# Performance work log

Measured on AMD Instinct MI355X. Metric: run time of the kernel, lower is better.

## Reference

```python
import jax, jax.numpy as jnp
import numpy as np

B, T, E, H = 4, 1024, 512, 8
DH = E // H  # head dim = 64


def setup_inputs() -> dict:
    key = jax.random.key(0)
    ks = jax.random.split(key, 6)
    s = 1.0 / np.sqrt(E)
    return {
        "q": jax.random.normal(ks[0], (B, T, E), dtype=jnp.float32),
        "kv": jax.random.normal(ks[1], (B, T, E), dtype=jnp.float32),
        "Wq": jax.random.normal(ks[2], (E, E), dtype=jnp.float32) * s,
        "Wk": jax.random.normal(ks[3], (E, E), dtype=jnp.float32) * s,
        "Wv": jax.random.normal(ks[4], (E, E), dtype=jnp.float32) * s,
        "Wo": jax.random.normal(ks[5], (E, E), dtype=jnp.float32) * s,
        "head_num": H,
    }


def _split_heads_dh(x, h):
    # einops 'b t (d h)' with h=head_num: head index is FASTEST in channel dim
    b, t, e = x.shape
    d = e // h
    return x.reshape(b, t, d, h).transpose(0, 3, 1, 2)  # (b, h, t, d)


def reference(q, kv, Wq, Wk, Wv, Wo, head_num):
    e = q.shape[-1]
    dk = (e // head_num) ** 0.5  # NOTE: multiplied, per original code

    qp = q @ Wq   # weights stored as (in, out); Linear(bias=False)
    kp = kv @ Wk
    vp = kv @ Wv

    query = _split_heads_dh(qp, head_num)  # (b, h, t, d)
    key = _split_heads_dh(kp, head_num)
    value = _split_heads_dh(vp, head_num)

    qf = jnp.fft.fftn(query, axes=(-2, -1))  # complex, over (t, d)
    kf = jnp.fft.fftn(key, axes=(-2, -1))

    # complex einsum, key NOT conjugated (faithful to torch source)
    energy = jnp.einsum("bhid,bhjd->bhij", qf, kf) * dk
    energy = jnp.fft.ifftn(energy, axes=(-2, -1)).real  # (b, h, t, t)

    attention = jax.nn.softmax(energy, axis=-1)
    out = jnp.einsum("bhij,bhjd->bhid", attention, value)  # (b, h, t, d)

    # einops 'b h t d -> b t (h d)': head index SLOWEST in output channel dim
    b, h, t, d = out.shape
    out = out.transpose(0, 2, 1, 3).reshape(b, t, h * d)
    return out @ Wo
```

## Files before the change

### kernel.cpp

```cpp
#include <hip/hip_runtime.h>
#include <math.h>

#define BB 4
#define TT 1024
#define EE 512
#define HH 8
#define DD 64
#define BT (BB * TT)

typedef _Float16 f16;
typedef __attribute__((ext_vector_type(8))) _Float16 f16x8;
typedef __attribute__((ext_vector_type(4))) float f32x4;

__global__ __launch_bounds__(256) void prep_k(
    const float* __restrict__ q, const float* __restrict__ kv,
    const float* __restrict__ Wq, const float* __restrict__ Wk,
    const float* __restrict__ Wv, const float* __restrict__ Wo,
    f16* __restrict__ wqh, f16* __restrict__ wql,
    f16* __restrict__ wkh, f16* __restrict__ wkl,
    f16* __restrict__ wvh, f16* __restrict__ woh,
    f16* __restrict__ qAhi, f16* __restrict__ qAlo,
    f16* __restrict__ kvAhi, f16* __restrict__ kvAlo) {
    const int t = threadIdx.x;
    const int y = blockIdx.y;
    if (y < 4) {
        int idx = blockIdx.x * 256 + t;
        int k = idx & (EE - 1);
        int n = idx >> 9;
        if (y == 0) {
            float v = Wq[k * EE + n] * 512.0f;
            f16 hi = (f16)v;
            wqh[n * EE + k] = hi;
            wql[n * EE + k] = (f16)(v - (float)hi);
        } else if (y == 1) {
            int d = n >> 3, h = n & 7;
            int sn = (((DD - d) & (DD - 1)) << 3) | h;
            float v = Wk[k * EE + sn];
            f16 hi = (f16)v;
            wkh[n * EE + k] = hi;
            wkl[n * EE + k] = (f16)(v - (float)hi);
        } else if (y == 2) {
            wvh[n * EE + k] = (f16)Wv[k * EE + n];
        } else {
            woh[n * EE + k] = (f16)Wo[k * EE + n];
        }
    } else {
        const float* src = (y == 4) ? q : kv;
        f16* dh = (y == 4) ? qAhi : kvAhi;
        f16* dl = (y == 4) ? qAlo : kvAlo;
        int base = (blockIdx.x * 256 + t) * 8;
        float4 a = *(const float4*)&src[base];
        float4 c = *(const float4*)&src[base + 4];
        float xs[8] = {a.x, a.y, a.z, a.w, c.x, c.y, c.z, c.w};
        f16x8 hi, lo;
#pragma unroll
        for (int e = 0; e < 8; ++e) {
            f16 hh = (f16)xs[e];
            hi[e] = hh;
            lo[e] = (f16)(xs[e] - (float)hh);
        }
        *(f16x8*)&dh[base] = hi;
        *(f16x8*)&dl[base] = lo;
    }
}

__global__ __launch_bounds__(256) void proj_k(
    const f16* __restrict__ qAhi, const f16* __restrict__ qAlo,
    const f16* __restrict__ kvAhi, const f16* __restrict__ kvAlo,
    const f16* __restrict__ wqh, const f16* __restrict__ wql,
    const f16* __restrict__ wkh, const f16* __restrict__ wkl,
    const f16* __restrict__ wvh,
    f16* __restrict__ qhi, f16* __restrict__ qlo,
    f16* __restrict__ khi, f16* __restrict__ klo, f16* __restrict__ vP) {
    __shared__ __align__(16) f16 Ah_s[2][128][40];
    __shared__ __align__(16) f16 Al_s[2][128][40];
    __shared__ __align__(16) f16 Wh_s[2][64][40];
    __shared__ __align__(16) f16 Wl_s[2][64][40];
    __shared__ __align__(16) f16 Wv_s[2][64][40];
    f16 (*Ep)[136] = reinterpret_cast<f16(*)[136]>(&Ah_s[0][0][0]);

    const int t = threadIdx.x;
    const int w = t >> 6, l = t & 63;
    const int wm = w >> 1, wn = w & 1;
    const int fr = l & 15, fc = l >> 4;
    const int m0b = blockIdx.x * 128;
    const int n0b = blockIdx.y * 64;
    const int z   = blockIdx.z;
    const int ar = t >> 1, ak = t & 1;
    const int wr = t >> 2, wc = t & 3;

    const f16* AH = z ? kvAhi : qAhi;
    const f16* AL = z ? kvAlo : qAlo;
    const f16* WH = z ? wkh : wqh;
    const f16* WL = z ? wkl : wql;

    f32x4 accK[4][2], accV[4][2];
#pragma unroll
    for (int i = 0; i < 4; ++i)
#pragma unroll
        for (int j = 0; j < 2; ++j) {
            accK[i][j] = f32x4{0.f, 0.f, 0.f, 0.f};
            accV[i][j] = f32x4{0.f, 0.f, 0.f, 0.f};
        }

    f16x8 ah8[2], al8[2], wh8, wl8, wv8;

    auto loadAB = [&](int k0) {
        size_t aoff = (size_t)(m0b + ar) * EE + k0 + ak * 16;
        ah8[0] = *(const f16x8*)&AH[aoff];
        ah8[1] = *(const f16x8*)&AH[aoff + 8];
        al8[0] = *(const f16x8*)&AL[aoff];
        al8[1] = *(const f16x8*)&AL[aoff + 8];
        size_t woff = (size_t)(n0b + wr) * EE + k0 + wc * 8;
        wh8 = *(const f16x8*)&WH[woff];
        wl8 = *(const f16x8*)&WL[woff];
        if (z) wv8 = *(const f16x8*)&wvh[woff];
    };
    auto stage = [&](int bf) {
        *(f16x8*)&Ah_s[bf][ar][ak * 16]     = ah8[0];
        *(f16x8*)&Ah_s[bf][ar][ak * 16 + 8] = ah8[1];
        *(f16x8*)&Al_s[bf][ar][ak * 16]     = al8[0];
        *(f16x8*)&Al_s[bf][ar][ak * 16 + 8] = al8[1];
        *(f16x8*)&Wh_s[bf][wr][wc * 8] = wh8;
        *(f16x8*)&Wl_s[bf][wr][wc * 8] = wl8;
        if (z) *(f16x8*)&Wv_s[bf][wr][wc * 8] = wv8;
    };

    loadAB(0);
    stage(0);
    __syncthreads();
    int cur = 0;
    for (int ks = 0; ks < 16; ++ks) {
        if (ks < 15) loadAB((ks + 1) * 32);
        f16x8 Ahf[4], Alf[4], Bh[2], Bl[2], Bv[2];
#pragma unroll
        for (int mi = 0; mi < 4; ++mi) {
            Ahf[mi] = *(const f16x8*)&Ah_s[cur][wm * 64 + mi * 16 + fr][fc * 8];
            Alf[mi] = *(const f16x8*)&Al_s[cur][wm * 64 + mi * 16 + fr][fc * 8];
        }
#pragma unroll
        for (int nj = 0; nj < 2; ++nj) {
            Bh[nj] = *(const f16x8*)&Wh_s[cur][wn * 32 + nj * 16 + fr][fc * 8];
            Bl[nj] = *(const f16x8*)&Wl_s[cur][wn * 32 + nj * 16 + fr][fc * 8];
            if (z) Bv[nj] = *(const f16x8*)&Wv_s[cur][wn * 32 + nj * 16 + fr][fc * 8];
        }
        __builtin_amdgcn_s_setprio(1);
#pragma unroll
        for (int mi = 0; mi < 4; ++mi)
#pragma unroll
            for (int nj = 0; nj < 2; ++nj) {
                accK[mi][nj] = __builtin_amdgcn_mfma_f32_16x16x32_f16(
                    Ahf[mi], Bh[nj], accK[mi][nj], 0, 0, 0);
                accK[mi][nj] = __builtin_amdgcn_mfma_f32_16x16x32_f16(
                    Ahf[mi], Bl[nj], accK[mi][nj], 0, 0, 0);
                accK[mi][nj] = __builtin_amdgcn_mfma_f32_16x16x32_f16(
                    Alf[mi], Bh[nj], accK[mi][nj], 0, 0, 0);
                if (z)
                    accV[mi][nj] = __builtin_amdgcn_mfma_f32_16x16x32_f16(
                        Ahf[mi], Bv[nj], accV[mi][nj], 0, 0, 0);
            }
        __builtin_amdgcn_s_setprio(0);
        if (ks < 15) stage(cur ^ 1);
        __syncthreads();
        cur ^= 1;
    }

    f16* dsthi = z ? khi : qhi;
    f16* dstlo = z ? klo : qlo;
#pragma unroll
    for (int mi = 0; mi < 4; ++mi)
#pragma unroll
        for (int nj = 0; nj < 2; ++nj)
#pragma unroll
            for (int r = 0; r < 4; ++r)
                Ep[wn * 32 + nj * 16 + fr][wm * 64 + mi * 16 + fc * 4 + r] =
                    (f16)accK[mi][nj][r];
    __syncthreads();
#pragma unroll
    for (int i = 0; i < 4; ++i) {
        int task = t * 4 + i;
        int mr = task >> 3, h = task & 7;
        f16x8 v;
#pragma unroll
        for (int d = 0; d < 8; ++d) v[d] = Ep[8 * d + h][mr];
        *(f16x8*)&dsthi[((size_t)h * BT + m0b + mr) * DD + (n0b >> 3)] = v;
    }
    __syncthreads();
#pragma unroll
    for (int mi = 0; mi < 4; ++mi)
#pragma unroll
        for (int nj = 0; nj < 2; ++nj)
#pragma unroll
            for (int r = 0; r < 4; ++r) {
                float x = accK[mi][nj][r];
                f16 hh = (f16)x;
                Ep[wn * 32 + nj * 16 + fr][wm * 64 + mi * 16 + fc * 4 + r] =
                    (f16)(x - (float)hh);
            }
    __syncthreads();
#pragma unroll
    for (int i = 0; i < 4; ++i) {
        int task = t * 4 + i;
        int mr = task >> 3, h = task & 7;
        f16x8 v;
#pragma unroll
        for (int d = 0; d < 8; ++d) v[d] = Ep[8 * d + h][mr];
        *(f16x8*)&dstlo[((size_t)h * BT + m0b + mr) * DD + (n0b >> 3)] = v;
    }
    if (z) {
        __syncthreads();
#pragma unroll
        for (int mi = 0; mi < 4; ++mi)
#pragma unroll
            for (int nj = 0; nj < 2; ++nj)
#pragma unroll
                for (int r = 0; r < 4; ++r)
                    Ep[wn * 32 + nj * 16 + fr][wm * 64 + mi * 16 + fc * 4 + r] =
                        (f16)accV[mi][nj][r];
        __syncthreads();
#pragma unroll
        for (int i = 0; i < 4; ++i) {
            int task = t * 4 + i;
            int mg = task & 15, nn = task >> 4;
            int h = nn & 7, dl = nn >> 3;
            int d = (n0b >> 3) + dl;
            int koff = m0b + mg * 8;
            int tile = koff >> 6;
            int kf   = (koff >> 5) & 1;
            int lg2  = (koff >> 3) & 3;
            int dvt  = d >> 4, lqd = d & 15;
            f16x8 v = *(const f16x8*)&Ep[nn][mg * 8];
            size_t off = (((((size_t)h * 64 + tile) * 2 + kf) * 4 + dvt) * 64 +
                          lg2 * 16 + lqd) * 8;
            *(f16x8*)&vP[off] = v;
        }
    }
}

__global__ __launch_bounds__(256) void outmm_k(const f16* __restrict__ Af,
                                               const f16* __restrict__ WThi,
                                               float* __restrict__ out) {
    __shared__ __align__(16) f16 Ah_s[2][64][72];
    __shared__ __align__(16) f16 Wh_s[2][64][72];

    const int t = threadIdx.x;
    const int w = t >> 6, l = t & 63;
    const int wm = w >> 1, wn = w & 1;
    const int fr = l & 15, fc = l >> 4;
    const int m0b = blockIdx.x * 64;
    const int n0b = blockIdx.y * 64;
    const int sr = t >> 2, sch = t & 3;

    f32x4 acc[2][2];
#pragma unroll
    for (int i = 0; i < 2; ++i)
#pragma unroll
        for (int j = 0; j < 2; ++j) acc[i][j] = f32x4{0.f, 0.f, 0.f, 0.f};

    f16x8 af[2], wf[2];
    auto loadAB = [&](int k0) {
#pragma unroll
        for (int i = 0; i < 2; ++i) {
            af[i] = *(const f16x8*)&Af[(size_t)(m0b + sr) * EE + k0 + sch * 16 + i * 8];
            wf[i] = *(const f16x8*)&WThi[(size_t)(n0b + sr) * EE + k0 + sch * 16 + i * 8];
        }
    };
    auto stage = [&](int bf) {
#pragma unroll
        for (int i = 0; i < 2; ++i) {
            *(f16x8*)&Ah_s[bf][sr][sch * 16 + i * 8] = af[i];
            *(f16x8*)&Wh_s[bf][sr][sch * 16 + i * 8] = wf[i];
        }
    };

    loadAB(0);
    stage(0);
    __syncthreads();
    int cur = 0;
    for (int ks = 0; ks < 8; ++ks) {
        if (ks < 7) loadAB((ks + 1) * 64);
        f16x8 Ahf[2][2], Bhf[2][2];
#pragma unroll
        for (int mi = 0; mi < 2; ++mi)
#pragma unroll
            for (int kb = 0; kb < 2; ++kb)
                Ahf[mi][kb] =
                    *(const f16x8*)&Ah_s[cur][wm * 32 + mi * 16 + fr][kb * 32 + fc * 8];
#pragma unroll
        for (int nj = 0; nj < 2; ++nj)
#pragma unroll
            for (int kb = 0; kb < 2; ++kb)
                Bhf[nj][kb] =
                    *(const f16x8*)&Wh_s[cur][wn * 32 + nj * 16 + fr][kb * 32 + fc * 8];
        __builtin_amdgcn_s_setprio(1);
#pragma unroll
        for (int mi = 0; mi < 2; ++mi)
#pragma unroll
            for (int nj = 0; nj < 2; ++nj)
#pragma unroll
                for (int kb = 0; kb < 2; ++kb)
                    acc[mi][nj] = __builtin_amdgcn_mfma_f32_16x16x32_f16(
                        Ahf[mi][kb], Bhf[nj][kb], acc[mi][nj], 0, 0, 0);
        __builtin_amdgcn_s_setprio(0);
        if (ks < 7) stage(cur ^ 1);
        __syncthreads();
        cur ^= 1;
    }

#pragma unroll
    for (int mi = 0; mi < 2; ++mi)
#pragma unroll
        for (int nj = 0; nj < 2; ++nj)
#pragma unroll
            for (int r = 0; r < 4; ++r)
                out[(size_t)(m0b + wm * 32 + mi * 16 + fc * 4 + r) * EE +
                    n0b + wn * 32 + nj * 16 + fr] = acc[mi][nj][r];
}

__global__ __launch_bounds__(256) void attn_mfma_k(const f16* __restrict__ qhiP,
    const f16* __restrict__ qloP, const f16* __restrict__ khiP,
    const f16* __restrict__ kloP, const f16* __restrict__ vP,
    f16* __restrict__ ctx) {
    __shared__ __align__(16) f16 Khi[2][64][64];
    __shared__ __align__(16) f16 Klo[2][64][64];
    __shared__ __align__(16) f16 Pl[4][16][88];

    const int bid = blockIdx.x;
    const int swz = (bid & 7) * 64 + (bid >> 3);
    const int bx = swz & 15;
    const int h  = (swz >> 4) & 7;
    const int b  = swz >> 7;

    const int t  = threadIdx.x;
    const int w  = t >> 6;
    const int l  = t & 63;
    const int lg = l >> 4;
    const int lq = l & 15;
    const int q0 = bx * 64 + w * 16;
    const size_t plane = ((size_t)h * BT + (size_t)b * TT) * DD;

    f16x8 Qhi[2], Qlo[2];
#pragma unroll
    for (int kf = 0; kf < 2; ++kf) {
        size_t qo = plane + (size_t)(q0 + lq) * DD + kf * 32 + lg * 8;
        Qhi[kf] = *(const f16x8*)&qhiP[qo];
        Qlo[kf] = *(const f16x8*)&qloP[qo];
    }

    f32x4 Oacc[4];
#pragma unroll
    for (int i = 0; i < 4; ++i) Oacc[i] = f32x4{0.f, 0.f, 0.f, 0.f};
    float m = -1e30f, lsum = 0.f;

    const int sr = t >> 2, sch = t & 3;
    f16x8 kh[2], kl[2];

    auto loadK = [&](int kt0) {
        size_t off = plane + (size_t)(kt0 + sr) * DD + sch * 16;
        kh[0] = *(const f16x8*)&khiP[off];
        kh[1] = *(const f16x8*)&khiP[off + 8];
        kl[0] = *(const f16x8*)&kloP[off];
        kl[1] = *(const f16x8*)&kloP[off + 8];
    };
    auto stageK = [&](int bf) {
#pragma unroll
        for (int i = 0; i < 2; ++i) {
            int chunk = sch * 2 + i;
            int dsw = chunk ^ (sr & 7);
            *(f16x8*)&Khi[bf][sr][dsw * 8] = kh[i];
            *(f16x8*)&Klo[bf][sr][dsw * 8] = kl[i];
        }
    };

    loadK(0);
    stageK(0);
    __syncthreads();
    int cur = 0;

    for (int kt0 = 0; kt0 < TT; kt0 += 64) {
        const f16* tb = vP + ((size_t)h * 64 + ((b * TT + kt0) >> 6)) * 4096;
        f16x8 bv[2][4];
#pragma unroll
        for (int kf = 0; kf < 2; ++kf)
#pragma unroll
            for (int dvt = 0; dvt < 4; ++dvt)
                bv[kf][dvt] = *(const f16x8*)&tb[((kf * 4 + dvt) * 64 + l) * 8];
        if (kt0 + 64 < TT) loadK(kt0 + 64);

        f32x4 Sc[4];
        __builtin_amdgcn_s_setprio(1);
#pragma unroll
        for (int kt = 0; kt < 4; ++kt) {
            f32x4 c = f32x4{0.f, 0.f, 0.f, 0.f};
            int keyr = kt * 16 + lq;
#pragma unroll
            for (int kf = 0; kf < 2; ++kf) {
                int dblk = kf * 4 + lg;
                int sw = dblk ^ (keyr & 7);
                f16x8 ahi = *(const f16x8*)&Khi[cur][keyr][sw * 8];
                f16x8 alo = *(const f16x8*)&Klo[cur][keyr][sw * 8];
                c = __builtin_amdgcn_mfma_f32_16x16x32_f16(ahi, Qhi[kf], c, 0, 0, 0);
                c = __builtin_amdgcn_mfma_f32_16x16x32_f16(ahi, Qlo[kf], c, 0, 0, 0);
                c = __builtin_amdgcn_mfma_f32_16x16x32_f16(alo, Qhi[kf], c, 0, 0, 0);
            }
            Sc[kt] = c;
        }
        __builtin_amdgcn_s_setprio(0);

        float sv[16];
#pragma unroll
        for (int kt = 0; kt < 4; ++kt)
#pragma unroll
            for (int r = 0; r < 4; ++r) sv[kt * 4 + r] = Sc[kt][r];
        float tm = sv[0];
#pragma unroll
        for (int i = 1; i < 16; ++i) tm = fmaxf(tm, sv[i]);
        tm = fmaxf(tm, __shfl_xor(tm, 16));
        tm = fmaxf(tm, __shfl_xor(tm, 32));

        bool skip = __all(tm <= m + 8.0f);
        float Mn = m, corr = 1.0f;
        if (!skip) {
            Mn = fmaxf(m, tm);
            corr = __expf(m - Mn);
        }
        float ps = 0.f;
        f16 ph[16];
#pragma unroll
        for (int i = 0; i < 16; ++i) {
            float p = __expf(sv[i] - Mn);
            ps += p;
            ph[i] = (f16)p;
        }
        ps += __shfl_xor(ps, 16);
        ps += __shfl_xor(ps, 32);
        if (skip) {
            lsum += ps;
        } else {
            lsum = lsum * corr + ps;
            m = Mn;
        }

#pragma unroll
        for (int kt = 0; kt < 4; ++kt)
#pragma unroll
            for (int rp = 0; rp < 4; rp += 2) {
                union { f16 h; unsigned short u; } u0, u1;
                u0.h = ph[kt * 4 + rp]; u1.h = ph[kt * 4 + rp + 1];
                unsigned int pk = ((unsigned int)u1.u << 16) | u0.u;
                *(unsigned int*)&Pl[w][lq][kt * 16 + lg * 4 + rp] = pk;
            }

        if (!skip) {
            float cq[4];
#pragma unroll
            for (int r = 0; r < 4; ++r) cq[r] = __shfl(corr, lg * 4 + r);
#pragma unroll
            for (int dvt = 0; dvt < 4; ++dvt)
#pragma unroll
                for (int r = 0; r < 4; ++r) Oacc[dvt][r] *= cq[r];
        }

        __builtin_amdgcn_s_setprio(1);
#pragma unroll
        for (int kf = 0; kf < 2; ++kf) {
            f16x8 pa = *(const f16x8*)&Pl[w][lq][kf * 32 + lg * 8];
#pragma unroll
            for (int dvt = 0; dvt < 4; ++dvt)
                Oacc[dvt] = __builtin_amdgcn_mfma_f32_16x16x32_f16(
                    pa, bv[kf][dvt], Oacc[dvt], 0, 0, 0);
        }
        __builtin_amdgcn_s_setprio(0);

        if (kt0 + 64 < TT) stageK(cur ^ 1);
        __syncthreads();
        cur ^= 1;
    }

    float linv = 1.0f / lsum;
    float lq4[4];
#pragma unroll
    for (int r = 0; r < 4; ++r) lq4[r] = __shfl(linv, lg * 4 + r);
#pragma unroll
    for (int r = 0; r < 4; ++r) {
        f16* crow = ctx + (size_t)(b * TT + q0 + lg * 4 + r) * EE + h * DD;
#pragma unroll
        for (int dvt = 0; dvt < 4; ++dvt)
            crow[dvt * 16 + lq] = (f16)(Oacc[dvt][r] * lq4[r]);
    }
}

extern "C" void kernel_launch(void* const* d_in, const int* in_sizes, int n_in,
                              void* d_out, int out_size, void* d_ws, size_t ws_size,
                              hipStream_t stream) {
    const float* q  = (const float*)d_in[0];
    const float* kv = (const float*)d_in[1];
    const float* Wq = (const float*)d_in[2];
    const float* Wk = (const float*)d_in[3];
    const float* Wv = (const float*)d_in[4];
    const float* Wo = (const float*)d_in[5];
    float* out = (float*)d_out;

    f16* ws = (f16*)d_ws;
    const size_t PL  = (size_t)HH * BT * DD;
    const size_t WPL = (size_t)EE * EE;
    f16* qhi   = ws + 0 * PL;
    f16* qlo   = ws + 1 * PL;
    f16* khi   = ws + 2 * PL;
    f16* klo   = ws + 3 * PL;
    f16* vPck  = ws + 4 * PL;
    f16* ctx   = ws + 5 * PL;
    f16* qAhi  = ws + 6 * PL;
    f16* qAlo  = ws + 7 * PL;
    f16* kvAhi = ws + 8 * PL;
    f16* kvAlo = ws + 9 * PL;
    f16* wqh = ws + 10 * PL;
    f16* wql = wqh + 1 * WPL;
    f16* wkh = wqh + 2 * WPL;
    f16* wkl = wqh + 3 * WPL;
    f16* wvh = wqh + 4 * WPL;
    f16* woh = wqh + 5 * WPL;

    prep_k<<<dim3(1024, 6), dim3(256), 0, stream>>>(
        q, kv, Wq, Wk, Wv, Wo, wqh, wql, wkh, wkl, wvh, woh,
        qAhi, qAlo, kvAhi, kvAlo);

    proj_k<<<dim3(BT / 128, EE / 64, 2), dim3(256), 0, stream>>>(
        qAhi, qAlo, kvAhi, kvAlo, wqh, wql, wkh, wkl, wvh,
        qhi, qlo, khi, klo, vPck);

    attn_mfma_k<<<dim3(512), dim3(256), 0, stream>>>(
        qhi, qlo, khi, klo, vPck, ctx);

    outmm_k<<<dim3(BT / 64, EE / 64), dim3(256), 0, stream>>>(ctx, woh, out);
}
```

Baseline: 77.08 us.

## Deepen software pipelining in projection GEMM and attention loops

The projection GEMM loop now keeps two register sets of prefetched tiles, so global loads run two k-steps ahead of the shared-memory stage, and the loop is unrolled by two with fixed buffer indices. The attention loop is restructured so the QK^T MFMAs for the next key tile are issued before the softmax and PV of the current tile, and V fragments are double-buffered in registers. The aim is to hide global-memory latency and overlap the score MFMAs with softmax ALU work. The cost is higher register pressure, which may lower occupancy or cause spills.

```diff
diff --git a/kernel.cpp b/kernel.cpp
--- a/kernel.cpp
+++ b/kernel.cpp
@@ -103,46 +103,43 @@
             accV[i][j] = f32x4{0.f, 0.f, 0.f, 0.f};
         }
 
-    f16x8 ah8[2], al8[2], wh8, wl8, wv8;
-
-    auto loadAB = [&](int k0) {
+    f16x8 ahA[2], alA[2], whA, wlA, wvA;
+    f16x8 ahB[2], alB[2], whB, wlB, wvB;
+
+    auto loadSet = [&](int k0, f16x8 (&ah)[2], f16x8 (&al)[2],
+                       f16x8& wh, f16x8& wl, f16x8& wv) {
         size_t aoff = (size_t)(m0b + ar) * EE + k0 + ak * 16;
-        ah8[0] = *(const f16x8*)&AH[aoff];
-        ah8[1] = *(const f16x8*)&AH[aoff + 8];
-        al8[0] = *(const f16x8*)&AL[aoff];
-        al8[1] = *(const f16x8*)&AL[aoff + 8];
+        ah[0] = *(const f16x8*)&AH[aoff];
+        ah[1] = *(const f16x8*)&AH[aoff + 8];
+        al[0] = *(const f16x8*)&AL[aoff];
+        al[1] = *(const f16x8*)&AL[aoff + 8];
         size_t woff = (size_t)(n0b + wr) * EE + k0 + wc * 8;
-        wh8 = *(const f16x8*)&WH[woff];
-        wl8 = *(const f16x8*)&WL[woff];
-        if (z) wv8 = *(const f16x8*)&wvh[woff];
-    };
-    auto stage = [&](int bf) {
-        *(f16x8*)&Ah_s[bf][ar][ak * 16]     = ah8[0];
-        *(f16x8*)&Ah_s[bf][ar][ak * 16 + 8] = ah8[1];
-        *(f16x8*)&Al_s[bf][ar][ak * 16]     = al8[0];
-        *(f16x8*)&Al_s[bf][ar][ak * 16 + 8] = al8[1];
-        *(f16x8*)&Wh_s[bf][wr][wc * 8] = wh8;
-        *(f16x8*)&Wl_s[bf][wr][wc * 8] = wl8;
-        if (z) *(f16x8*)&Wv_s[bf][wr][wc * 8] = wv8;
-    };
-
-    loadAB(0);
-    stage(0);
-    __syncthreads();
-    int cur = 0;
-    for (int ks = 0; ks < 16; ++ks) {
-        if (ks < 15) loadAB((ks + 1) * 32);
+        wh = *(const f16x8*)&WH[woff];
+        wl = *(const f16x8*)&WL[woff];
+        if (z) wv = *(const f16x8*)&wvh[woff];
+    };
+    auto stageSet = [&](int bf, f16x8 (&ah)[2], f16x8 (&al)[2],
+                        f16x8& wh, f16x8& wl, f16x8& wv) {
+        *(f16x8*)&Ah_s[bf][ar][ak * 16]     = ah[0];
+        *(f16x8*)&Ah_s[bf][ar][ak * 16 + 8] = ah[1];
+        *(f16x8*)&Al_s[bf][ar][ak * 16]     = al[0];
+        *(f16x8*)&Al_s[bf][ar][ak * 16 + 8] = al[1];
+        *(f16x8*)&Wh_s[bf][wr][wc * 8] = wh;
+        *(f16x8*)&Wl_s[bf][wr][wc * 8] = wl;
+        if (z) *(f16x8*)&Wv_s[bf][wr][wc * 8] = wv;
+    };
+    auto comp = [&](int bf) {
         f16x8 Ahf[4], Alf[4], Bh[2], Bl[2], Bv[2];
 #pragma unroll
         for (int mi = 0; mi < 4; ++mi) {
-            Ahf[mi] = *(const f16x8*)&Ah_s[cur][wm * 64 + mi * 16 + fr][fc * 8];
-            Alf[mi] = *(const f16x8*)&Al_s[cur][wm * 64 + mi * 16 + fr][fc * 8];
+            Ahf[mi] = *(const f16x8*)&Ah_s[bf][wm * 64 + mi * 16 + fr][fc * 8];
+            Alf[mi] = *(const f16x8*)&Al_s[bf][wm * 64 + mi * 16 + fr][fc * 8];
         }
 #pragma unroll
         for (int nj = 0; nj < 2; ++nj) {
-            Bh[nj] = *(const f16x8*)&Wh_s[cur][wn * 32 + nj * 16 + fr][fc * 8];
-            Bl[nj] = *(const f16x8*)&Wl_s[cur][wn * 32 + nj * 16 + fr][fc * 8];
-            if (z) Bv[nj] = *(const f16x8*)&Wv_s[cur][wn * 32 + nj * 16 + fr][fc * 8];
+            Bh[nj] = *(const f16x8*)&Wh_s[bf][wn * 32 + nj * 16 + fr][fc * 8];
+            Bl[nj] = *(const f16x8*)&Wl_s[bf][wn * 32 + nj * 16 + fr][fc * 8];
+            if (z) Bv[nj] = *(const f16x8*)&Wv_s[bf][wn * 32 + nj * 16 + fr][fc * 8];
         }
         __builtin_amdgcn_s_setprio(1);
 #pragma unroll
@@ -160,9 +157,23 @@
                         Ahf[mi], Bv[nj], accV[mi][nj], 0, 0, 0);
             }
         __builtin_amdgcn_s_setprio(0);
-        if (ks < 15) stage(cur ^ 1);
+    };
+
+    loadSet(0, ahA, alA, whA, wlA, wvA);
+    stageSet(0, ahA, alA, whA, wlA, wvA);
+    loadSet(32, ahA, alA, whA, wlA, wvA);
+    loadSet(64, ahB, alB, whB, wlB, wvB);
+    __syncthreads();
+
+    for (int ks = 0; ks < 16; ks += 2) {
+        comp(0);
+        stageSet(1, ahA, alA, whA, wlA, wvA);
+        if (ks + 3 < 16) loadSet((ks + 3) * 32, ahA, alA, whA, wlA, wvA);
         __syncthreads();
-        cur ^= 1;
+        comp(1);
+        if (ks + 2 < 16) stageSet(0, ahB, alB, whB, wlB, wvB);
+        if (ks + 4 < 16) loadSet((ks + 4) * 32, ahB, alB, whB, wlB, wvB);
+        __syncthreads();
     }
 
     f16* dsthi = z ? khi : qhi;
@@ -372,22 +383,18 @@
         }
     };
 
-    loadK(0);
-    stageK(0);
-    __syncthreads();
-    int cur = 0;
-
-    for (int kt0 = 0; kt0 < TT; kt0 += 64) {
+    f16x8 bvA[2][4], bvB[2][4];
+    auto loadBV = [&](int kt0, f16x8 (&bv)[2][4]) {
         const f16* tb = vP + ((size_t)h * 64 + ((b * TT + kt0) >> 6)) * 4096;
-        f16x8 bv[2][4];
 #pragma unroll
         for (int kf = 0; kf < 2; ++kf)
 #pragma unroll
             for (int dvt = 0; dvt < 4; ++dvt)
                 bv[kf][dvt] = *(const f16x8*)&tb[((kf * 4 + dvt) * 64 + l) * 8];
-        if (kt0 + 64 < TT) loadK(kt0 + 64);
-
-        f32x4 Sc[4];
+    };
+
+    f32x4 ScA[4], ScB[4];
+    auto QK = [&](int curb, f32x4 (&Sc)[4]) {
         __builtin_amdgcn_s_setprio(1);
 #pragma unroll
         for (int kt = 0; kt < 4; ++kt) {
@@ -395,10 +402,9 @@
             int keyr = kt * 16 + lq;
 #pragma unroll
             for (int kf = 0; kf < 2; ++kf) {
-                int dblk = kf * 4 + lg;
-                int sw = dblk ^ (keyr & 7);
-                f16x8 ahi = *(const f16x8*)&Khi[cur][keyr][sw * 8];
-                f16x8 alo = *(const f16x8*)&Klo[cur][keyr][sw * 8];
+                int sw = (kf * 4 + lg) ^ (keyr & 7);
+                f16x8 ahi = *(const f16x8*)&Khi[curb][keyr][sw * 8];
+                f16x8 alo = *(const f16x8*)&Klo[curb][keyr][sw * 8];
                 c = __builtin_amdgcn_mfma_f32_16x16x32_f16(ahi, Qhi[kf], c, 0, 0, 0);
                 c = __builtin_amdgcn_mfma_f32_16x16x32_f16(ahi, Qlo[kf], c, 0, 0, 0);
                 c = __builtin_amdgcn_mfma_f32_16x16x32_f16(alo, Qhi[kf], c, 0, 0, 0);
@@ -406,7 +412,9 @@
             Sc[kt] = c;
         }
         __builtin_amdgcn_s_setprio(0);
-
+    };
+
+    auto SMPV = [&](const f32x4 (&Sc)[4], const f16x8 (&bv)[2][4]) {
         float sv[16];
 #pragma unroll
         for (int kt = 0; kt < 4; ++kt)
@@ -471,10 +479,31 @@
                     pa, bv[kf][dvt], Oacc[dvt], 0, 0, 0);
         }
         __builtin_amdgcn_s_setprio(0);
-
-        if (kt0 + 64 < TT) stageK(cur ^ 1);
+    };
+
+    loadK(0);
+    stageK(0);
+    loadK(64);
+    loadBV(0, bvA);
+    __syncthreads();
+    QK(0, ScA);
+    stageK(1);
+    __syncthreads();
+
+    for (int t2 = 0; t2 < 16; t2 += 2) {
+        const int kt0 = t2 << 6;
+        loadBV(kt0 + 64, bvB);
+        if (t2 + 2 < 16) loadK(kt0 + 128);
+        QK(1, ScB);
+        SMPV(ScA, bvA);
+        if (t2 + 2 < 16) stageK(0);
         __syncthreads();
-        cur ^= 1;
+        if (t2 + 2 < 16) loadBV(kt0 + 128, bvA);
+        if (t2 + 3 < 16) loadK(kt0 + 192);
+        if (t2 + 2 < 16) QK(0, ScA);
+        SMPV(ScB, bvB);
+        if (t2 + 3 < 16) stageK(1);
+        if (t2 + 2 < 16) __syncthreads();
     }
 
     float linv = 1.0f / lsum;
```

Result: no change. 78.00 us (+1.2%).
